# Optimization experiments

Hardware: AMD Instinct MI355X
Metric: run time of the kernel (lower is better)

Reference implementation:

```python
import jax, jax.numpy as jnp
import numpy as np

V, E, H, T = 100000, 128, 256, 7
B, S = 64, 512
START, STOP = 5, 6
H2 = H // 2


def setup_inputs() -> dict:
    key = jax.random.key(0)
    ks = jax.random.split(key, 16)
    rn = lambda k, shape, s=0.1: jax.random.normal(k, shape, jnp.float32) * s
    inp = {}
    inp["sentence"] = jax.random.randint(ks[0], (B, S), 0, V)
    inp["tags"] = jax.random.randint(ks[1], (B, S), 0, 5)
    inp["h0"] = jax.random.normal(ks[2], (2, B, H2), jnp.float32)
    inp["c0"] = jax.random.normal(ks[3], (2, B, H2), jnp.float32)
    inp["embedding"] = rn(ks[4], (V, E), 1.0)
    inp["w_ih_f"] = rn(ks[5], (4 * H2, E)); inp["w_hh_f"] = rn(ks[6], (4 * H2, H2))
    inp["b_ih_f"] = rn(ks[7], (4 * H2,)); inp["b_hh_f"] = rn(ks[8], (4 * H2,))
    inp["w_ih_b"] = rn(ks[9], (4 * H2, E)); inp["w_hh_b"] = rn(ks[10], (4 * H2, H2))
    inp["b_ih_b"] = rn(ks[11], (4 * H2,)); inp["b_hh_b"] = rn(ks[12], (4 * H2,))
    inp["w_out"] = rn(ks[13], (T, H)); inp["b_out"] = rn(ks[14], (T,))
    trans = jax.random.normal(ks[15], (T, T), jnp.float32)
    trans = trans.at[START, :].set(-10000.0).at[:, STOP].set(-10000.0)
    inp["transitions"] = trans
    return inp


def _lstm_dir(x, h0, c0, wih, whh, bih, bhh, reverse):
    # x: [S, B, E]; PyTorch gate order i, f, g, o
    def step(carry, xt):
        h, c = carry
        z = xt @ wih.T + h @ whh.T + bih + bhh  # [B, 4*H2]
        i, f, g, o = jnp.split(z, 4, axis=-1)
        c = jax.nn.sigmoid(f) * c + jax.nn.sigmoid(i) * jnp.tanh(g)
        h = jax.nn.sigmoid(o) * jnp.tanh(c)
        return (h, c), h
    _, hs = jax.lax.scan(step, (h0, c0), x, reverse=reverse)
    return hs  # [S, B, H2]


def reference(sentence, tags, h0, c0, embedding, w_ih_f, w_hh_f, b_ih_f, b_hh_f,
              w_ih_b, w_hh_b, b_ih_b, b_hh_b, w_out, b_out, transitions):
    # Embedding; torch code does .view(S, B, -1) on a [B, S, E] tensor (raw
    # reinterpretation) -- replicate with reshape to match the math exactly.
    embeds = embedding[sentence].reshape(S, B, E)
    hf = _lstm_dir(embeds, h0[0], c0[0], w_ih_f, w_hh_f, b_ih_f, b_hh_f, False)
    hb = _lstm_dir(embeds, h0[1], c0[1], w_ih_b, w_hh_b, b_ih_b, b_hh_b, True)
    feats = jnp.concatenate([hf, hb], axis=-1) @ w_out.T + b_out  # [S, B, T]

    # CRF forward algorithm. Original uses transitions.t(), i.e. step score
    # for prev=i -> next=j is transitions[i, j].
    alpha0 = jnp.full((B, T), -10000.0, jnp.float32).at[:, START].set(0.0)
    def crf_step(alpha, feat):
        # [b, i, j]: alpha[b,i] + transitions[i,j]; LSE over i, add emit[b,j]
        a = jax.nn.logsumexp(alpha[:, :, None] + transitions[None, :, :], axis=1) + feat
        return a, None
    alpha, _ = jax.lax.scan(crf_step, alpha0, feats)
    fwd_score = jax.nn.logsumexp(alpha + transitions[STOP][None, :], axis=1)  # [B]

    # Gold path score: transitions[next, prev] + emit[next], per _score_sentence.
    tags_ext = jnp.concatenate([jnp.full((B, 1), START, tags.dtype), tags], axis=1)
    t_prev, t_next = tags_ext[:, :-1], tags_ext[:, 1:]  # [B, S]
    trans_sc = transitions[t_next, t_prev].sum(axis=1)
    emit_sc = jnp.take_along_axis(jnp.transpose(feats, (1, 0, 2)),
                                  t_next[:, :, None], axis=2)[..., 0].sum(axis=1)
    gold = trans_sc + emit_sc + transitions[STOP, tags_ext[:, -1]]
    return jnp.sum(fwd_score - gold) / B
```

## Files before the change

kernel.cpp:

```cpp
#include <hip/hip_runtime.h>

typedef unsigned int u32;
typedef unsigned short u16;
typedef __attribute__((ext_vector_type(8))) short short8;
typedef __attribute__((ext_vector_type(4))) float f32x4;
typedef __attribute__((ext_vector_type(2))) float f32x2;

#define DEV __device__ __forceinline__
#define LOG2E 1.44269504089f

DEV u16 f2bf(float f) {
    u32 u = __float_as_uint(f);
    return (u16)((u + 0x7FFFu + ((u >> 16) & 1u)) >> 16);
}
DEV float bf2f(u16 h) { return __uint_as_float(((u32)h) << 16); }
DEV float frcp(float x) { return __builtin_amdgcn_rcpf(x); }
DEV float fexp2(float x) {
#if __has_builtin(__builtin_amdgcn_exp2f)
    return __builtin_amdgcn_exp2f(x);
#else
    return exp2f(x);
#endif
}
DEV u32 pack_bf16(float a, float b) {
#if __has_builtin(__builtin_amdgcn_cvt_pk_bf16_f32)
    auto v = __builtin_amdgcn_cvt_pk_bf16_f32(a, b);
    u32 r; __builtin_memcpy(&r, &v, 4); return r;
#else
    return (u32)f2bf(a) | ((u32)f2bf(b) << 16);
#endif
}
DEV float xex(uint2 v, int r) {
    u32 u = (r & 2) ? v.y : v.x;
    return (r & 1) ? __uint_as_float(u & 0xFFFF0000u) : __uint_as_float(u << 16);
}

DEV f32x2 exp2p(f32x2 a) { f32x2 r; r.x = fexp2(a.x); r.y = fexp2(a.y); return r; }
DEV f32x2 rcpp(f32x2 a)  { f32x2 r; r.x = frcp(a.x);  r.y = frcp(a.y);  return r; }
DEV f32x2 minp(f32x2 a, float b) { f32x2 r; r.x = fminf(a.x, b); r.y = fminf(a.y, b); return r; }
DEV f32x2 LOp(f32x4 v) { f32x2 r; r.x = v[0]; r.y = v[1]; return r; }
DEV f32x2 HIp(f32x4 v) { f32x2 r; r.x = v[2]; r.y = v[3]; return r; }

DEV f32x2 lstm_pair(f32x2 zi, f32x2 zf, f32x2 zg, f32x2 zo, f32x2* cst) {
    f32x2 ei = exp2p(-zi);
    f32x2 ef = exp2p(-zf);
    f32x2 eo = exp2p(-zo);
    f32x2 eg = exp2p(minp(zg + zg, 115.f));
    f32x2 A = 1.f + ei, F = 1.f + ef, G = eg + 1.f, O = 1.f + eo;
    f32x2 AG = A * G;
    f32x2 cc = (*cst * AG + (eg - 1.f) * F) * rcpp(F * AG);
    *cst = cc;
    f32x2 ec = exp2p(minp(cc * 2.885390082f, 115.f));
    return (ec - 1.f) * rcpp(O * (ec + 1.f));
}

__global__ __launch_bounds__(512) void k_inproj2(
    const int* __restrict__ sent, const float* __restrict__ emb,
    const float* __restrict__ wihf, const float* __restrict__ bihf, const float* __restrict__ bhhf,
    const float* __restrict__ wihb, const float* __restrict__ bihb, const float* __restrict__ bhhb,
    u16* __restrict__ Xf, u16* __restrict__ Xb)
{
    int blk = blockIdx.x;
    int d  = blk >> 7;
    int sc = blk & 127;
    const float* wih = d ? wihb : wihf;
    const float* bih = d ? bihb : bihf;
    const float* bhh = d ? bhhb : bhhf;
    u16* X = d ? Xb : Xf;
    int tid = threadIdx.x;
    int w = tid >> 6, lane = tid & 63;
    int rg = lane >> 4, cn = lane & 15;

    short8 afr[4][4];
    #pragma unroll
    for (int mi = 0; mi < 4; ++mi) {
        int gate = 16 * (w + 8 * mi) + cn;
        #pragma unroll
        for (int kt = 0; kt < 4; ++kt) {
            const float* p = wih + (size_t)gate * 128 + kt * 32 + rg * 8;
            float4 f0 = *(const float4*)p;
            float4 f1 = *(const float4*)(p + 4);
            union { short8 v; u32 u[4]; } sv;
            sv.u[0] = pack_bf16(f0.x, f0.y);
            sv.u[1] = pack_bf16(f0.z, f0.w);
            sv.u[2] = pack_bf16(f1.x, f1.y);
            sv.u[3] = pack_bf16(f1.z, f1.w);
            afr[mi][kt] = sv.v;
        }
    }
    float bs[4][4];
    #pragma unroll
    for (int mi = 0; mi < 4; ++mi)
        #pragma unroll
        for (int r = 0; r < 4; ++r) {
            int g = 16 * (w + 8 * mi) + 4 * rg + r;
            bs[mi][r] = bih[g] + bhh[g];
        }

    __shared__ u16 tile[2][64][136];
    #pragma unroll
    for (int stage = 0; stage < 2; ++stage) {
        if (stage) __syncthreads();
        {
            int row = tid >> 2, q = tid & 3;
            int sl = row >> 6, bb = row & 63;
            int tok = sent[(sc * 4 + stage * 2 + sl) * 64 + bb];
            const float* er = emb + (size_t)tok * 128 + q * 32;
            u16* dst = &tile[sl][bb][q * 32];
            #pragma unroll
            for (int u = 0; u < 4; ++u) {
                float4 a = *(const float4*)(er + u * 8);
                float4 c = *(const float4*)(er + u * 8 + 4);
                uint4 st;
                st.x = pack_bf16(a.x, a.y); st.y = pack_bf16(a.z, a.w);
                st.z = pack_bf16(c.x, c.y); st.w = pack_bf16(c.z, c.w);
                *(uint4*)(dst + u * 8) = st;
            }
        }
        __syncthreads();
        #pragma unroll
        for (int ss = 0; ss < 2; ++ss) {
            int s = sc * 4 + stage * 2 + ss;
            #pragma unroll
            for (int nt = 0; nt < 4; ++nt) {
                short8 bfr[4];
                #pragma unroll
                for (int kt = 0; kt < 4; ++kt)
                    bfr[kt] = *(const short8*)&tile[ss][nt * 16 + cn][kt * 32 + rg * 8];
                #pragma unroll
                for (int mi = 0; mi < 4; ++mi) {
                    f32x4 acc = {0.f, 0.f, 0.f, 0.f};
                    #pragma unroll
                    for (int kt = 0; kt < 4; ++kt)
                        acc = __builtin_amdgcn_mfma_f32_16x16x32_bf16(afr[mi][kt], bfr[kt], acc, 0, 0, 0);
                    size_t base = (((size_t)s * 4 + nt) * 32 + (w + 8 * mi)) * 256
                                + (size_t)rg * 64 + (size_t)cn * 4;
                    uint2 st;
                    st.x = pack_bf16((acc[0] + bs[mi][0]) * LOG2E, (acc[1] + bs[mi][1]) * LOG2E);
                    st.y = pack_bf16((acc[2] + bs[mi][2]) * LOG2E, (acc[3] + bs[mi][3]) * LOG2E);
                    *(uint2*)(X + base) = st;
                }
            }
        }
    }
}

__global__ __launch_bounds__(512) void k_lstm(
    const float* __restrict__ h0, const float* __restrict__ c0,
    const float* __restrict__ whhf, const float* __restrict__ whhb,
    const u16* __restrict__ Xf, const u16* __restrict__ Xb,
    u16* __restrict__ hfo, u16* __restrict__ hbo)
{
    int d  = blockIdx.x >> 2, g4 = blockIdx.x & 3;
    const float* whh = d ? whhb : whhf;
    const u16*   X   = d ? Xb   : Xf;
    u16*         ho  = d ? hbo  : hfo;
    int w = threadIdx.x >> 6, lane = threadIdx.x & 63;
    int rg = lane >> 4, cn = lane & 15;

    short8 afr[4][4];
    #pragma unroll
    for (int mi = 0; mi < 4; ++mi) {
        int gate = 16 * (w + 8 * mi) + cn;
        #pragma unroll
        for (int kt = 0; kt < 4; ++kt) {
            const float* p = whh + (size_t)gate * 128 + kt * 32 + rg * 8;
            float4 f0 = *(const float4*)p;
            float4 f1 = *(const float4*)(p + 4);
            union { short8 v; u32 u[4]; } sv;
            sv.u[0] = pack_bf16(f0.x * LOG2E, f0.y * LOG2E);
            sv.u[1] = pack_bf16(f0.z * LOG2E, f0.w * LOG2E);
            sv.u[2] = pack_bf16(f1.x * LOG2E, f1.y * LOG2E);
            sv.u[3] = pack_bf16(f1.z * LOG2E, f1.w * LOG2E);
            afr[mi][kt] = sv.v;
        }
    }
    int b = g4 * 16 + cn;
    int chb = 16 * w + rg * 4;
    f32x2 cst01, cst23;
    {
        float4 cv = *(const float4*)(c0 + ((size_t)d * 64 + b) * 128 + chb);
        cst01.x = cv.x; cst01.y = cv.y;
        cst23.x = cv.z; cst23.y = cv.w;
    }
    __shared__ u16 hbuf[2][16][136];
    {
        float4 hv = *(const float4*)(h0 + ((size_t)d * 64 + b) * 128 + chb);
        uint2 st0;
        st0.x = pack_bf16(hv.x, hv.y);
        st0.y = pack_bf16(hv.z, hv.w);
        *(uint2*)&hbuf[0][cn][chb] = st0;
    }
    __syncthreads();

    int s0 = d ? 511 : 0;
    const int sdelta = d ? -32768 : 32768;
    const ptrdiff_t hdelta = d ? -8192 : 8192;
    size_t lof = (size_t)rg * 64 + (size_t)cn * 4;

    const u16* pa[4]; const u16* pb[4];
    uint2 xA[4], xB[4];
    #pragma unroll
    for (int mi = 0; mi < 4; ++mi) {
        const u16* base = X + (((size_t)s0 * 4 + g4) * 32 + (w + 8 * mi)) * 256 + lof;
        xA[mi] = *(const uint2*)base;
        xB[mi] = *(const uint2*)(base + sdelta);
        pa[mi] = base + 2 * sdelta;
        pb[mi] = base + 3 * sdelta;
    }
    u16* hop = ho + ((size_t)s0 * 64 + b) * 128 + chb;

#define LSTM_STEP(RB, WB, XC, XP)                                            \
    do {                                                                     \
        short8 bfr[4];                                                       \
        _Pragma("unroll")                                                    \
        for (int kt = 0; kt < 4; ++kt)                                       \
            bfr[kt] = *(const short8*)&hbuf[RB][cn][kt * 32 + rg * 8];       \
        f32x4 z[4];                                                          \
        _Pragma("unroll")                                                    \
        for (int mi = 0; mi < 4; ++mi) {                                     \
            f32x4 acc;                                                       \
            acc[0] = xex(XC[mi], 0); acc[1] = xex(XC[mi], 1);                \
            acc[2] = xex(XC[mi], 2); acc[3] = xex(XC[mi], 3);                \
            _Pragma("unroll")                                                \
            for (int kt = 0; kt < 4; ++kt)                                   \
                acc = __builtin_amdgcn_mfma_f32_16x16x32_bf16(               \
                    afr[mi][kt], bfr[kt], acc, 0, 0, 0);                     \
            z[mi] = acc;                                                     \
            XC[mi] = *(const uint2*)XP[mi];                                  \
            XP[mi] += 2 * sdelta;                                            \
        }                                                                    \
        f32x2 h01 = lstm_pair(LOp(z[0]), LOp(z[1]),                          \
                              LOp(z[2]), LOp(z[3]), &cst01);                 \
        f32x2 h23 = lstm_pair(HIp(z[0]), HIp(z[1]),                          \
                              HIp(z[2]), HIp(z[3]), &cst23);                 \
        uint2 st;                                                            \
        st.x = pack_bf16(h01.x, h01.y);                                      \
        st.y = pack_bf16(h23.x, h23.y);                                      \
        *(uint2*)&hbuf[WB][cn][chb] = st;                                    \
        *(uint2*)hop = st;                                                   \
        hop += hdelta;                                                       \
        asm volatile("s_waitcnt lgkmcnt(0)\n\ts_barrier" ::: "memory");      \
    } while (0)

    for (int it = 0; it < 256; ++it) {
        LSTM_STEP(0, 1, xA, pa);
        LSTM_STEP(1, 0, xB, pb);
    }
#undef LSTM_STEP
}

__global__ __launch_bounds__(256) void k_feats(
    const u16* __restrict__ hf, const u16* __restrict__ hb,
    const float* __restrict__ wout, const float* __restrict__ bout,
    float* __restrict__ feats)
{
    __shared__ u16 sf[32][136], sb[32][136];
    __shared__ float wo[7][260];
    __shared__ float bo[8];
    int tid = threadIdx.x;
    int pos0 = blockIdx.x * 32;
    {
        int r = tid >> 3, cc = (tid & 7) * 16;
        const uint4* pf = (const uint4*)(hf + (size_t)(pos0 + r) * 128 + cc);
        const uint4* pb = (const uint4*)(hb + (size_t)(pos0 + r) * 128 + cc);
        *(uint4*)&sf[r][cc]     = pf[0];
        *(uint4*)&sf[r][cc + 8] = pf[1];
        *(uint4*)&sb[r][cc]     = pb[0];
        *(uint4*)&sb[r][cc + 8] = pb[1];
    }
    for (int i = tid; i < 1792; i += 256) wo[i >> 8][i & 255] = wout[i];
    if (tid < 7) bo[tid] = bout[tid];
    __syncthreads();
    int pp = tid >> 3, tt = tid & 7;
    if (tt < 7) {
        float acc = bo[tt];
        #pragma unroll 4
        for (int ch = 0; ch < 128; ++ch)
            acc += bf2f(sf[pp][ch]) * wo[tt][ch]
                 + bf2f(sb[pp][ch]) * wo[tt][128 + ch];
        feats[(size_t)(pos0 + pp) * 7 + tt] = acc;
    }
}

__global__ __launch_bounds__(64) void k_crf_chunk(
    const float* __restrict__ feats, const float* __restrict__ trans,
    float* __restrict__ chunkM)
{
    int b = blockIdx.x >> 3, c = blockIdx.x & 7;
    int lane = threadIdx.x;
    int i = lane >> 3, j = lane & 7;
    __shared__ float M[8][8];
    __shared__ float fl[64][8];
    int s0 = c * 64;
    for (int idx = lane; idx < 448; idx += 64) {
        int ss = idx / 7, jj = idx - ss * 7;
        fl[ss][jj] = feats[(size_t)((s0 + ss) * 64 + b) * 7 + jj];
    }
    float tc[7];
    #pragma unroll
    for (int k = 0; k < 7; ++k) tc[k] = (j < 7) ? trans[k * 7 + j] : 0.f;
    __syncthreads();
    M[i][j] = (i < 7 && j < 7) ? (trans[i * 7 + j] + fl[0][j]) : -1e30f;
    __syncthreads();
    for (int ss = 1; ss < 64; ++ss) {
        float4 m0 = *(const float4*)&M[i][0];
        float4 m1 = *(const float4*)&M[i][4];
        float v0 = m0.x + tc[0], v1 = m0.y + tc[1], v2 = m0.z + tc[2];
        float v3 = m0.w + tc[3], v4 = m1.x + tc[4], v5 = m1.y + tc[5];
        float v6 = m1.z + tc[6];
        float mx = fmaxf(fmaxf(fmaxf(v0, v1), fmaxf(v2, v3)),
                         fmaxf(fmaxf(v4, v5), v6));
        float sm = __expf(v0 - mx) + __expf(v1 - mx) + __expf(v2 - mx)
                 + __expf(v3 - mx) + __expf(v4 - mx) + __expf(v5 - mx)
                 + __expf(v6 - mx);
        float r = mx + __logf(sm) + fl[ss][j];
        __syncthreads();
        if (i < 7 && j < 7) M[i][j] = r;
        __syncthreads();
    }
    if (i < 7 && j < 7)
        chunkM[(size_t)(b * 8 + c) * 49 + i * 7 + j] = M[i][j];
}

__global__ __launch_bounds__(512) void k_crf_final(
    const float* __restrict__ chunkM, const float* __restrict__ trans,
    const int* __restrict__ tags, const float* __restrict__ feats,
    float* __restrict__ out)
{
    int tid = threadIdx.x;
    int w = tid >> 6, lane = tid & 63;
    int k = lane >> 3, j = lane & 7;
    int b = w * 8 + k;
    bool jv = (j < 7);
    __shared__ float Tl[49];
    __shared__ float red[512];
    __shared__ float fsh[64];
    if (tid < 49) Tl[tid] = trans[tid];
    __syncthreads();

    float av = (j == 5) ? 0.f : -1e4f;
    #pragma unroll
    for (int c = 0; c < 8; ++c) {
        float a0 = __shfl(av, k * 8 + 0, 64);
        float a1 = __shfl(av, k * 8 + 1, 64);
        float a2 = __shfl(av, k * 8 + 2, 64);
        float a3 = __shfl(av, k * 8 + 3, 64);
        float a4 = __shfl(av, k * 8 + 4, 64);
        float a5 = __shfl(av, k * 8 + 5, 64);
        float a6 = __shfl(av, k * 8 + 6, 64);
        if (jv) {
            const float* Pp = chunkM + ((size_t)b * 8 + c) * 49 + j;
            float v0 = a0 + Pp[0],  v1 = a1 + Pp[7],  v2 = a2 + Pp[14];
            float v3 = a3 + Pp[21], v4 = a4 + Pp[28], v5 = a5 + Pp[35];
            float v6 = a6 + Pp[42];
            float mx = fmaxf(fmaxf(fmaxf(v0, v1), fmaxf(v2, v3)),
                             fmaxf(fmaxf(v4, v5), v6));
            float sm = __expf(v0 - mx) + __expf(v1 - mx) + __expf(v2 - mx)
                     + __expf(v3 - mx) + __expf(v4 - mx) + __expf(v5 - mx)
                     + __expf(v6 - mx);
            av = mx + __logf(sm);
        }
    }
    float u = jv ? (av + Tl[42 + j]) : -1e30f;
    float m = u;
    #pragma unroll
    for (int off = 1; off < 8; off <<= 1) m = fmaxf(m, __shfl_xor(m, off, 64));
    float e = jv ? __expf(u - m) : 0.f;
    #pragma unroll
    for (int off = 1; off < 8; off <<= 1) e += __shfl_xor(e, off, 64);
    float fwd = m + __logf(e);
    if (j == 0) fsh[b] = fwd;

    int tb = tid & 63, q = tid >> 6;
    const int* tgp = tags + (size_t)tb * 512;
    float acc = 0.f;
    int tp = (q == 0) ? 5 : tgp[q * 64 - 1];
    for (int ss = q * 64; ss < q * 64 + 64; ++ss) {
        int tn = tgp[ss];
        acc += Tl[tn * 7 + tp] + feats[(size_t)(ss * 64 + tb) * 7 + tn];
        tp = tn;
    }
    if (q == 7) acc += Tl[42 + tgp[511]];
    red[tid] = acc;
    __syncthreads();
    if (tid < 64) {
        float g = red[tid];
        #pragma unroll
        for (int qq = 1; qq < 8; ++qq) g += red[tid + 64 * qq];
        red[tid] = fsh[tid] - g;
    }
    __syncthreads();
    if (tid < 64) {
        float v = red[tid];
        #pragma unroll
        for (int off = 1; off < 64; off <<= 1) v += __shfl_xor(v, off, 64);
        if (tid == 0) out[0] = v * (1.0f / 64.0f);
    }
}

extern "C" void kernel_launch(void* const* d_in, const int* in_sizes, int n_in,
                              void* d_out, int out_size, void* d_ws, size_t ws_size,
                              hipStream_t stream) {
    const int*   sent = (const int*)d_in[0];
    const int*   tags = (const int*)d_in[1];
    const float* h0   = (const float*)d_in[2];
    const float* c0   = (const float*)d_in[3];
    const float* emb  = (const float*)d_in[4];
    const float* wihf = (const float*)d_in[5];
    const float* whhf = (const float*)d_in[6];
    const float* bihf = (const float*)d_in[7];
    const float* bhhf = (const float*)d_in[8];
    const float* wihb = (const float*)d_in[9];
    const float* whhb = (const float*)d_in[10];
    const float* bihb = (const float*)d_in[11];
    const float* bihb2 = bihb; (void)bihb2;
    const float* bhhb = (const float*)d_in[12];
    const float* wout = (const float*)d_in[13];
    const float* bout = (const float*)d_in[14];
    const float* trn  = (const float*)d_in[15];

    char* ws = (char*)d_ws;
    u16*   Xf     = (u16*)(ws);
    u16*   Xb     = (u16*)(ws + 33554432);
    u16*   hfp    = (u16*)(ws + 67108864);
    u16*   hbp    = (u16*)(ws + 75497472);
    float* feats  = (float*)(ws + 83886080);
    float* chunkM = (float*)(ws + 84803584);

    k_inproj2<<<256, 512, 0, stream>>>(sent, emb, wihf, bihf, bhhf,
                                       wihb, bihb, bhhb, Xf, Xb);
    k_lstm<<<8, 512, 0, stream>>>(h0, c0, whhf, whhb, Xf, Xb, hfp, hbp);
    k_feats<<<1024, 256, 0, stream>>>(hfp, hbp, wout, bout, feats);
    k_crf_chunk<<<512, 64, 0, stream>>>(feats, trn, chunkM);
    k_crf_final<<<1, 512, 0, stream>>>(chunkM, trn, tags, feats, (float*)d_out);
}
```

Baseline: 573.2 us.

## Interleave LSTM gate rows so each lane holds i,f,g,o of one channel

Remaps the gate ordering (gmap) in both the input projection and recurrent weights so that each MFMA output fragment row group contains the i, f, g, o gates for the same hidden channel. In the recurrent loop this lets each lane compute cell updates for two channel pairs directly from its accumulators, with no cross-lane dependence. The trade-off is that hidden-state writes become strided 16-bit stores to LDS and global memory instead of one packed 8-byte store. It also vectorizes the bf16 reads in the feats projection kernel.

```diff
diff --git a/kernel.cpp b/kernel.cpp
--- a/kernel.cpp
+++ b/kernel.cpp
@@ -35,11 +35,11 @@
     return (r & 1) ? __uint_as_float(u & 0xFFFF0000u) : __uint_as_float(u << 16);
 }
 
+DEV int gmap(int g) { return (g & 3) * 128 + (g >> 2); }
+
 DEV f32x2 exp2p(f32x2 a) { f32x2 r; r.x = fexp2(a.x); r.y = fexp2(a.y); return r; }
 DEV f32x2 rcpp(f32x2 a)  { f32x2 r; r.x = frcp(a.x);  r.y = frcp(a.y);  return r; }
 DEV f32x2 minp(f32x2 a, float b) { f32x2 r; r.x = fminf(a.x, b); r.y = fminf(a.y, b); return r; }
-DEV f32x2 LOp(f32x4 v) { f32x2 r; r.x = v[0]; r.y = v[1]; return r; }
-DEV f32x2 HIp(f32x4 v) { f32x2 r; r.x = v[2]; r.y = v[3]; return r; }
 
 DEV f32x2 lstm_pair(f32x2 zi, f32x2 zf, f32x2 zg, f32x2 zo, f32x2* cst) {
     f32x2 ei = exp2p(-zi);
@@ -74,7 +74,7 @@
     short8 afr[4][4];
     #pragma unroll
     for (int mi = 0; mi < 4; ++mi) {
-        int gate = 16 * (w + 8 * mi) + cn;
+        int gate = gmap(16 * (w + 8 * mi) + cn);
         #pragma unroll
         for (int kt = 0; kt < 4; ++kt) {
             const float* p = wih + (size_t)gate * 128 + kt * 32 + rg * 8;
@@ -93,7 +93,7 @@
     for (int mi = 0; mi < 4; ++mi)
         #pragma unroll
         for (int r = 0; r < 4; ++r) {
-            int g = 16 * (w + 8 * mi) + 4 * rg + r;
+            int g = gmap(16 * (w + 8 * mi) + 4 * rg + r);
             bs[mi][r] = bih[g] + bhh[g];
         }
 
@@ -161,7 +161,7 @@
     short8 afr[4][4];
     #pragma unroll
     for (int mi = 0; mi < 4; ++mi) {
-        int gate = 16 * (w + 8 * mi) + cn;
+        int gate = gmap(16 * (w + 8 * mi) + cn);
         #pragma unroll
         for (int kt = 0; kt < 4; ++kt) {
             const float* p = whh + (size_t)gate * 128 + kt * 32 + rg * 8;
@@ -176,15 +176,15 @@
         }
     }
     int b = g4 * 16 + cn;
-    int chb = 16 * w + rg * 4;
-    f32x2 cst01, cst23;
+    int ch0 = 4 * w + rg;
+    f32x2 cstA, cstB;
     {
-        float4 cv = *(const float4*)(c0 + ((size_t)d * 64 + b) * 128 + chb);
-        cst01.x = cv.x; cst01.y = cv.y;
-        cst23.x = cv.z; cst23.y = cv.w;
+        const float* cp = c0 + ((size_t)d * 64 + b) * 128 + ch0;
+        cstA.x = cp[0]; cstA.y = cp[32]; cstB.x = cp[64]; cstB.y = cp[96];
     }
     __shared__ u16 hbuf[2][16][136];
     {
+        int chb = 16 * w + rg * 4;
         float4 hv = *(const float4*)(h0 + ((size_t)d * 64 + b) * 128 + chb);
         uint2 st0;
         st0.x = pack_bf16(hv.x, hv.y);
@@ -208,7 +208,7 @@
         pa[mi] = base + 2 * sdelta;
         pb[mi] = base + 3 * sdelta;
     }
-    u16* hop = ho + ((size_t)s0 * 64 + b) * 128 + chb;
+    u16* hop = ho + ((size_t)s0 * 64 + b) * 128 + ch0;
 
 #define LSTM_STEP(RB, WB, XC, XP)                                            \
     do {                                                                     \
@@ -230,15 +230,19 @@
             XC[mi] = *(const uint2*)XP[mi];                                  \
             XP[mi] += 2 * sdelta;                                            \
         }                                                                    \
-        f32x2 h01 = lstm_pair(LOp(z[0]), LOp(z[1]),                          \
-                              LOp(z[2]), LOp(z[3]), &cst01);                 \
-        f32x2 h23 = lstm_pair(HIp(z[0]), HIp(z[1]),                          \
-                              HIp(z[2]), HIp(z[3]), &cst23);                 \
-        uint2 st;                                                            \
-        st.x = pack_bf16(h01.x, h01.y);                                      \
-        st.y = pack_bf16(h23.x, h23.y);                                      \
-        *(uint2*)&hbuf[WB][cn][chb] = st;                                    \
-        *(uint2*)hop = st;                                                   \
+        f32x2 ziA = {z[0][0], z[1][0]}, zfA = {z[0][1], z[1][1]};            \
+        f32x2 zgA = {z[0][2], z[1][2]}, zoA = {z[0][3], z[1][3]};            \
+        f32x2 hA = lstm_pair(ziA, zfA, zgA, zoA, &cstA);                     \
+        f32x2 ziB = {z[2][0], z[3][0]}, zfB = {z[2][1], z[3][1]};            \
+        f32x2 zgB = {z[2][2], z[3][2]}, zoB = {z[2][3], z[3][3]};            \
+        f32x2 hB = lstm_pair(ziB, zfB, zgB, zoB, &cstB);                     \
+        u32 pAw = pack_bf16(hA.x, hA.y);                                     \
+        u32 pBw = pack_bf16(hB.x, hB.y);                                     \
+        u16* hb = &hbuf[WB][cn][ch0];                                        \
+        hb[0]  = (u16)pAw; hb[32] = (u16)(pAw >> 16);                        \
+        hb[64] = (u16)pBw; hb[96] = (u16)(pBw >> 16);                        \
+        hop[0]  = (u16)pAw; hop[32] = (u16)(pAw >> 16);                      \
+        hop[64] = (u16)pBw; hop[96] = (u16)(pBw >> 16);                      \
         hop += hdelta;                                                       \
         asm volatile("s_waitcnt lgkmcnt(0)\n\ts_barrier" ::: "memory");      \
     } while (0)
@@ -276,9 +280,16 @@
     if (tt < 7) {
         float acc = bo[tt];
         #pragma unroll 4
-        for (int ch = 0; ch < 128; ++ch)
-            acc += bf2f(sf[pp][ch]) * wo[tt][ch]
-                 + bf2f(sb[pp][ch]) * wo[tt][128 + ch];
+        for (int ch = 0; ch < 128; ch += 2) {
+            u32 uf = *(const u32*)&sf[pp][ch];
+            u32 ub = *(const u32*)&sb[pp][ch];
+            float2 w0 = *(const float2*)&wo[tt][ch];
+            float2 w1 = *(const float2*)&wo[tt][128 + ch];
+            acc += __uint_as_float(uf << 16) * w0.x
+                 + __uint_as_float(uf & 0xFFFF0000u) * w0.y
+                 + __uint_as_float(ub << 16) * w1.x
+                 + __uint_as_float(ub & 0xFFFF0000u) * w1.y;
+        }
         feats[(size_t)(pos0 + pp) * 7 + tt] = acc;
     }
 }
@@ -414,7 +425,6 @@
     const float* wihb = (const float*)d_in[9];
     const float* whhb = (const float*)d_in[10];
     const float* bihb = (const float*)d_in[11];
-    const float* bihb2 = bihb; (void)bihb2;
     const float* bhhb = (const float*)d_in[12];
     const float* wout = (const float*)d_in[13];
     const float* bout = (const float*)d_in[14];
```

Measured after the change: 767.8 us. 1.34x slower.
